# Optimization experiments

Hardware: AMD Instinct MI355X
Metric: run time of the kernel (lower is better)

## Reference

```python
import jax, jax.numpy as jnp
import numpy as np

N, E, F_IN, HID, H1, H3, NC, G = 10000, 160000, 256, 128, 5, 3, 10, 64
NEG_SLOPE = 0.2  # PyG GATConv default


def _segment_softmax(e, seg, num_segments):
    # e: [E, H] edge logits, softmax over edges sharing the same destination
    m = jax.ops.segment_max(e, seg, num_segments=num_segments)  # [N, H]
    ex = jnp.exp(e - m[seg])
    s = jax.ops.segment_sum(ex, seg, num_segments=num_segments)
    return ex / (s[seg] + 1e-16)


def _gat_conv(x, src, dst, n, W, a_src, a_dst, b, concat):
    H, C = a_src.shape
    h = (x @ W).reshape(n, H, C)                 # per-head projected features
    al_s = (h * a_src).sum(-1)                   # [N, H]
    al_d = (h * a_dst).sum(-1)                   # [N, H]
    e = jax.nn.leaky_relu(al_s[src] + al_d[dst], NEG_SLOPE)   # [E, H]
    alpha = _segment_softmax(e, dst, n)
    out = jax.ops.segment_sum(alpha[:, :, None] * h[src], dst, num_segments=n)  # [N,H,C]
    out = out.reshape(n, H * C) if concat else out.mean(axis=1)
    return out + b


def setup_inputs():
    key = jax.random.key(0)
    ks = jax.random.split(key, 16)
    s = 0.1
    return {
        "x": jax.random.normal(ks[0], (N, F_IN), jnp.float32),
        "edge_index": jax.random.randint(ks[1], (2, E), 0, N),
        "batch": jnp.sort(jax.random.randint(ks[2], (N,), 0, G)),
        "W1": jax.random.normal(ks[3], (F_IN, H1 * HID), jnp.float32) * s,
        "a1s": jax.random.normal(ks[4], (H1, HID), jnp.float32) * s,
        "a1d": jax.random.normal(ks[5], (H1, HID), jnp.float32) * s,
        "b1": jnp.zeros((H1 * HID,), jnp.float32),
        "W2": jax.random.normal(ks[6], (H1 * HID, H1 * HID), jnp.float32) * s,
        "a2s": jax.random.normal(ks[7], (H1, HID), jnp.float32) * s,
        "a2d": jax.random.normal(ks[8], (H1, HID), jnp.float32) * s,
        "b2": jnp.zeros((H1 * HID,), jnp.float32),
        "W3": jax.random.normal(ks[9], (H1 * HID, H3 * HID), jnp.float32) * s,
        "a3s": jax.random.normal(ks[10], (H3, HID), jnp.float32) * s,
        "a3d": jax.random.normal(ks[11], (H3, HID), jnp.float32) * s,
        "b3": jnp.zeros((HID,), jnp.float32),
        "Wc": jax.random.normal(ks[12], (HID, NC), jnp.float32) * s,
        "bc": jnp.zeros((NC,), jnp.float32),
    }


def reference(x, edge_index, batch, W1, a1s, a1d, b1, W2, a2s, a2d, b2,
              W3, a3s, a3d, b3, Wc, bc):
    n = x.shape[0]
    # add self-loops (PyG GATConv default)
    loop = jnp.arange(n)
    src = jnp.concatenate([edge_index[0], loop])
    dst = jnp.concatenate([edge_index[1], loop])
    # dropout omitted: inference/eval mode
    x1 = jax.nn.elu(_gat_conv(x, src, dst, n, W1, a1s, a1d, b1, True))
    h = _gat_conv(x1, src, dst, n, W2, a2s, a2d, b2, True)
    x2 = jax.nn.elu(x1 + h)
    x3 = _gat_conv(x2, src, dst, n, W3, a3s, a3d, b3, False)  # concat=False -> head mean
    counts = jax.ops.segment_sum(jnp.ones((n,), x3.dtype), batch, num_segments=G)
    pooled = jax.ops.segment_sum(x3, batch, num_segments=G) / jnp.maximum(counts, 1.0)[:, None]
    logits = pooled @ Wc + bc
    return logits, jax.nn.log_softmax(logits, axis=1)
```

## Files before the change

kernel.cpp:

```cpp
#include <hip/hip_runtime.h>
#include <math.h>

#define NNODES 10000
#define NPAD   10112
#define NEDGES 160000
#define ETOT   170000
#define FIN    256
#define HIDC   128
#define NH1    5
#define NH3    3
#define NCLS   10
#define NG     64

typedef unsigned short u16;
typedef unsigned int   u32;
typedef __attribute__((ext_vector_type(8))) short short8;
typedef __attribute__((ext_vector_type(4))) float f32x4;

__device__ __forceinline__ u16 f2b(float f) {
    union { float f; u32 u; } v; v.f = f;
    u32 r = v.u + 0x7FFF + ((v.u >> 16) & 1);
    return (u16)(r >> 16);
}
__device__ __forceinline__ float b2f(u16 b) {
    union { u32 u; float f; } v; v.u = ((u32)b) << 16; return v.f;
}

__device__ __forceinline__ float wave_sum(float v) {
    #pragma unroll
    for (int m = 32; m; m >>= 1) v += __shfl_xor(v, m);
    return v;
}

__global__ void k_init(int* __restrict__ deg, int* __restrict__ cursor, int n) {
    int i = blockIdx.x * blockDim.x + threadIdx.x;
    if (i < n) { deg[i] = 1; cursor[i] = 0; }
}

__global__ void k_count(const int* __restrict__ dstv, int* __restrict__ deg, int E) {
    int e = blockIdx.x * blockDim.x + threadIdx.x;
    if (e < E) atomicAdd(&deg[dstv[e]], 1);
}

__global__ void k_scan(const int* __restrict__ deg, int* __restrict__ offs, int n) {
    __shared__ int wsum[4];
    __shared__ int carry_s;
    const int lane = threadIdx.x & 63, wave = threadIdx.x >> 6;
    if (threadIdx.x == 0) carry_s = 0;
    __syncthreads();
    for (int base = 0; base < n; base += 256) {
        int i = base + (int)threadIdx.x;
        int v = (i < n) ? deg[i] : 0;
        int xs = v;
        #pragma unroll
        for (int d = 1; d < 64; d <<= 1) {
            int y = __shfl_up(xs, d);
            if (lane >= d) xs += y;
        }
        if (lane == 63) wsum[wave] = xs;
        __syncthreads();
        int wadd = 0;
        for (int w = 0; w < wave; ++w) wadd += wsum[w];
        int incl = carry_s + wadd + xs;
        if (i < n) offs[i + 1] = incl;
        __syncthreads();
        if (threadIdx.x == 255) carry_s = incl;
        __syncthreads();
    }
    if (threadIdx.x == 0) offs[0] = 0;
}

__global__ void k_scatter(const int* __restrict__ srcv, const int* __restrict__ dstv,
                          const int* __restrict__ offs, int* __restrict__ cursor,
                          int* __restrict__ csr, int* __restrict__ dstc, int E, int N) {
    int e = blockIdx.x * blockDim.x + threadIdx.x;
    if (e >= E + N) return;
    int s, d;
    if (e < E) { s = srcv[e]; d = dstv[e]; }
    else       { s = d = e - E; }
    int pos = offs[d] + atomicAdd(&cursor[d], 1);
    csr[pos] = s;
    dstc[pos] = d;
}

__global__ void k_f2b4(const float4* __restrict__ X, uint2* __restrict__ Y, int n4) {
    int i = blockIdx.x * blockDim.x + threadIdx.x;
    if (i >= n4) return;
    float4 v = X[i];
    uint2 o;
    o.x = (u32)f2b(v.x) | ((u32)f2b(v.y) << 16);
    o.y = (u32)f2b(v.z) | ((u32)f2b(v.w) << 16);
    Y[i] = o;
}

__global__ void k_wt(const float* __restrict__ W, u16* __restrict__ Wt, int K, int Nw) {
    int i = blockIdx.x * blockDim.x + threadIdx.x;
    if (i >= K * Nw) return;
    int k = i / Nw, n = i - k * Nw;
    Wt[(size_t)n * K + k] = f2b(W[i]);
}

__global__ __launch_bounds__(256) void k_gemm_mfma(const u16* __restrict__ A,
                                                   const u16* __restrict__ Bt,
                                                   u16* __restrict__ C,
                                                   const float* __restrict__ a_s,
                                                   const float* __restrict__ a_d,
                                                   float* __restrict__ als,
                                                   float* __restrict__ ald,
                                                   int M, int K) {
    __shared__ __align__(16) u16 As[64 * 64];
    __shared__ __align__(16) u16 Bs[128 * 64];
    __shared__ float sAls[4][64];
    __shared__ float sAld[4][64];
    const int t = threadIdx.x;
    const int lane = t & 63, wave = t >> 6;
    const int row0 = blockIdx.x * 64;
    const int head = blockIdx.y;
    const int wn = wave * 32;
    const int frow = lane & 15, quad = lane >> 4;

    f32x4 acc[4][2];
    #pragma unroll
    for (int i = 0; i < 4; ++i)
        #pragma unroll
        for (int j = 0; j < 2; ++j)
            acc[i][j] = (f32x4){0.f, 0.f, 0.f, 0.f};

    const int srow = t >> 3;
    const int sg   = t & 7;

    short8 avec[2], bvec[4];
    #pragma unroll
    for (int i = 0; i < 2; ++i) {
        int r = srow + i * 32;
        avec[i] = *(const short8*)(A + (size_t)(row0 + r) * K + sg * 8);
    }
    #pragma unroll
    for (int i = 0; i < 4; ++i) {
        int r = srow + i * 32;
        bvec[i] = *(const short8*)(Bt + (size_t)(head * 128 + r) * K + sg * 8);
    }

    for (int k0 = 0; k0 < K; k0 += 64) {
        __syncthreads();
        #pragma unroll
        for (int i = 0; i < 2; ++i) {
            int r = srow + i * 32;
            *(short8*)(As + r * 64 + (sg ^ (r & 7)) * 8) = avec[i];
        }
        #pragma unroll
        for (int i = 0; i < 4; ++i) {
            int r = srow + i * 32;
            *(short8*)(Bs + r * 64 + (sg ^ (r & 7)) * 8) = bvec[i];
        }
        __syncthreads();
        if (k0 + 64 < K) {
            #pragma unroll
            for (int i = 0; i < 2; ++i) {
                int r = srow + i * 32;
                avec[i] = *(const short8*)(A + (size_t)(row0 + r) * K + k0 + 64 + sg * 8);
            }
            #pragma unroll
            for (int i = 0; i < 4; ++i) {
                int r = srow + i * 32;
                bvec[i] = *(const short8*)(Bt + (size_t)(head * 128 + r) * K + k0 + 64 + sg * 8);
            }
        }
        #pragma unroll
        for (int c = 0; c < 2; ++c) {
            short8 af[4], bfv[2];
            #pragma unroll
            for (int mi = 0; mi < 4; ++mi) {
                int rr = mi * 16 + frow;
                int g = (c * 4 + quad) ^ (rr & 7);
                af[mi] = *(const short8*)(As + rr * 64 + g * 8);
            }
            #pragma unroll
            for (int ni = 0; ni < 2; ++ni) {
                int rr = wn + ni * 16 + frow;
                int g = (c * 4 + quad) ^ (rr & 7);
                bfv[ni] = *(const short8*)(Bs + rr * 64 + g * 8);
            }
            #pragma unroll
            for (int mi = 0; mi < 4; ++mi)
                #pragma unroll
                for (int ni = 0; ni < 2; ++ni)
                    acc[mi][ni] = __builtin_amdgcn_mfma_f32_16x16x32_bf16(
                        af[mi], bfv[ni], acc[mi][ni], 0, 0, 0);
        }
    }
    u16* Ch = C + (size_t)head * NPAD * HIDC;
    float ps[16], pd[16];
    #pragma unroll
    for (int i = 0; i < 16; ++i) { ps[i] = 0.f; pd[i] = 0.f; }
    #pragma unroll
    for (int ni = 0; ni < 2; ++ni) {
        int col = wn + ni * 16 + frow;
        float as_c = a_s[head * HIDC + col];
        float ad_c = a_d[head * HIDC + col];
        #pragma unroll
        for (int mi = 0; mi < 4; ++mi) {
            #pragma unroll
            for (int r = 0; r < 4; ++r) {
                int row = row0 + mi * 16 + quad * 4 + r;
                u16 hb = f2b(acc[mi][ni][r]);
                if (row < M) Ch[(size_t)row * HIDC + col] = hb;
                float hv = b2f(hb);
                ps[mi * 4 + r] = fmaf(hv, as_c, ps[mi * 4 + r]);
                pd[mi * 4 + r] = fmaf(hv, ad_c, pd[mi * 4 + r]);
            }
        }
    }
    #pragma unroll
    for (int i = 0; i < 16; ++i) {
        #pragma unroll
        for (int msk = 1; msk < 16; msk <<= 1) {
            ps[i] += __shfl_xor(ps[i], msk);
            pd[i] += __shfl_xor(pd[i], msk);
        }
    }
    if (frow == 0) {
        #pragma unroll
        for (int mi = 0; mi < 4; ++mi)
            #pragma unroll
            for (int r = 0; r < 4; ++r) {
                sAls[wave][mi * 16 + quad * 4 + r] = ps[mi * 4 + r];
                sAld[wave][mi * 16 + quad * 4 + r] = pd[mi * 4 + r];
            }
    }
    __syncthreads();
    if (t < 64) {
        int row = row0 + t;
        if (row < M) {
            float vs = sAls[0][t] + sAls[1][t] + sAls[2][t] + sAls[3][t];
            float vd = sAld[0][t] + sAld[1][t] + sAld[2][t] + sAld[3][t];
            als[(size_t)head * NNODES + row] = vs;
            ald[(size_t)head * NNODES + row] = vd;
        }
    }
}

__global__ void k_elog(const float* __restrict__ als, const float* __restrict__ ald,
                       const int* __restrict__ csr, const int* __restrict__ dstc,
                       float* __restrict__ elog, int total) {
    int i = blockIdx.x * blockDim.x + threadIdx.x;
    if (i >= total) return;
    int hh = i / ETOT, e = i - hh * ETOT;
    int s = csr[e], d = dstc[e];
    float v = als[(size_t)hh * NNODES + s] + ald[(size_t)hh * NNODES + d];
    v = v > 0.f ? v : 0.2f * v;
    elog[i] = __expf(v);
}

template <int MODE>
__global__ __launch_bounds__(256) void k_agg(const u16* __restrict__ h,
                                             const float* __restrict__ elog,
                                             const int* __restrict__ offs,
                                             const int* __restrict__ csr,
                                             const float* __restrict__ bias,
                                             const float* __restrict__ residf,
                                             u16* __restrict__ outbf,
                                             float* __restrict__ outf, int NHtot) {
    const int b = blockIdx.x * 4 + (threadIdx.x >> 6);
    if (b >= NHtot) return;
    const int head = b / NNODES, n = b - head * NNODES;
    const int lane = threadIdx.x & 63;
    const int grp = lane >> 4;
    const int fl  = lane & 15;
    const int e0 = offs[n], e1 = offs[n + 1];
    const float* el = elog + (size_t)head * ETOT;
    const u16* hh = h + (size_t)head * NPAD * HIDC;

    float acc[8];
    #pragma unroll
    for (int i = 0; i < 8; ++i) acc[i] = 0.f;
    float wsum = 0.f;
    int e = e0 + grp;
    for (; e + 4 < e1; e += 8) {
        float w0 = el[e];
        float w1 = el[e + 4];
        int s0 = csr[e];
        int s1 = csr[e + 4];
        short8 hv0 = *(const short8*)(hh + (size_t)s0 * HIDC + fl * 8);
        short8 hv1 = *(const short8*)(hh + (size_t)s1 * HIDC + fl * 8);
        wsum += w0;
        #pragma unroll
        for (int i = 0; i < 8; ++i)
            acc[i] = fmaf(w0, b2f((u16)hv0[i]), acc[i]);
        wsum += w1;
        #pragma unroll
        for (int i = 0; i < 8; ++i)
            acc[i] = fmaf(w1, b2f((u16)hv1[i]), acc[i]);
    }
    for (; e < e1; e += 4) {
        float w = el[e];
        int s = csr[e];
        short8 hv = *(const short8*)(hh + (size_t)s * HIDC + fl * 8);
        wsum += w;
        #pragma unroll
        for (int i = 0; i < 8; ++i)
            acc[i] = fmaf(w, b2f((u16)hv[i]), acc[i]);
    }
    #pragma unroll
    for (int i = 0; i < 8; ++i) {
        acc[i] += __shfl_xor(acc[i], 16);
        acc[i] += __shfl_xor(acc[i], 32);
    }
    wsum += __shfl_xor(wsum, 16);
    wsum += __shfl_xor(wsum, 32);
    const float inv = 1.f / (wsum + 1e-16f);
    const int j0 = grp * 2;
    float v0 = acc[j0] * inv;
    float v1 = acc[j0 + 1] * inv;
    const int fo = fl * 8 + j0;
    if (MODE == 2) {
        *(float2*)(outf + ((size_t)head * NNODES + n) * HIDC + fo) = make_float2(v0, v1);
    } else {
        const int f0 = head * HIDC + fo;
        if (MODE == 1) {
            float2 r = *(const float2*)(residf + (size_t)n * 640 + f0);
            v0 = r.x + v0;
            v1 = r.y + v1;
        }
        v0 += bias[f0];
        v1 += bias[f0 + 1];
        v0 = v0 > 0.f ? v0 : expm1f(v0);
        v1 = v1 > 0.f ? v1 : expm1f(v1);
        *(u32*)(outbf + (size_t)n * 640 + f0) = (u32)f2b(v0) | ((u32)f2b(v1) << 16);
        if (MODE == 0)
            *(float2*)(outf + (size_t)n * 640 + f0) = make_float2(v0, v1);
    }
}

__global__ void k_mean_bias(const float* __restrict__ agg, const float* __restrict__ b,
                            float* __restrict__ o, int total) {
    int i = blockIdx.x * blockDim.x + threadIdx.x;
    if (i >= total) return;
    int n = i >> 7, c = i & 127;
    float v = (agg[((size_t)0 * NNODES + n) * HIDC + c] +
               agg[((size_t)1 * NNODES + n) * HIDC + c] +
               agg[((size_t)2 * NNODES + n) * HIDC + c]) * (1.f / 3.f) + b[c];
    o[i] = v;
}

__global__ void k_pool_zero(float* __restrict__ pooled, float* __restrict__ cnts) {
    int i = blockIdx.x * blockDim.x + threadIdx.x;
    if (i < NG * HIDC) pooled[i] = 0.f;
    if (i < NG) cnts[i] = 0.f;
}

#define PCHUNK 16
__global__ __launch_bounds__(128) void k_pool_chunk(const float* __restrict__ x3,
                                                    const int* __restrict__ batch,
                                                    float* __restrict__ pooled,
                                                    float* __restrict__ cnts, int N) {
    const int c  = threadIdx.x;
    const int n0 = blockIdx.x * PCHUNK;
    const int n1 = min(n0 + PCHUNK, N);
    int   cur = batch[n0];
    float acc = 0.f;
    int   cnt = 0;
    for (int n = n0; n < n1; ++n) {
        int g = batch[n];
        if (g != cur) {
            atomicAdd(&pooled[cur * HIDC + c], acc);
            if (c == 0) atomicAdd(&cnts[cur], (float)cnt);
            acc = 0.f; cnt = 0; cur = g;
        }
        acc += x3[(size_t)n * HIDC + c];
        ++cnt;
    }
    atomicAdd(&pooled[cur * HIDC + c], acc);
    if (c == 0) atomicAdd(&cnts[cur], (float)cnt);
}

__global__ void k_head(const float* __restrict__ pooled, const float* __restrict__ cnts,
                       const float* __restrict__ Wc, const float* __restrict__ bc,
                       float* __restrict__ out) {
    __shared__ float lg[NG][NCLS];
    int tid = threadIdx.x;
    if (tid < NG * NCLS) {
        int g = tid / NCLS, c = tid % NCLS;
        float invc = 1.f / fmaxf(cnts[g], 1.f);
        float s = bc[c];
        for (int k = 0; k < HIDC; ++k)
            s = fmaf(pooled[g * HIDC + k] * invc, Wc[k * NCLS + c], s);
        lg[g][c] = s;
        out[tid] = s;
    }
    __syncthreads();
    if (tid < NG * NCLS) {
        int g = tid / NCLS, c = tid % NCLS;
        float m = -1e30f;
        for (int j = 0; j < NCLS; ++j) m = fmaxf(m, lg[g][j]);
        float se = 0.f;
        for (int j = 0; j < NCLS; ++j) se += __expf(lg[g][j] - m);
        out[NG * NCLS + tid] = lg[g][c] - m - __logf(se);
    }
}

extern "C" void kernel_launch(void* const* d_in, const int* in_sizes, int n_in,
                              void* d_out, int out_size, void* d_ws, size_t ws_size,
                              hipStream_t stream) {
    const float* x   = (const float*)d_in[0];
    const int*   ei  = (const int*)d_in[1];
    const int*   bat = (const int*)d_in[2];
    const float* W1  = (const float*)d_in[3];
    const float* a1s = (const float*)d_in[4];
    const float* a1d = (const float*)d_in[5];
    const float* b1  = (const float*)d_in[6];
    const float* W2  = (const float*)d_in[7];
    const float* a2s = (const float*)d_in[8];
    const float* a2d = (const float*)d_in[9];
    const float* b2  = (const float*)d_in[10];
    const float* W3  = (const float*)d_in[11];
    const float* a3s = (const float*)d_in[12];
    const float* a3d = (const float*)d_in[13];
    const float* b3  = (const float*)d_in[14];
    const float* Wc  = (const float*)d_in[15];
    const float* bc  = (const float*)d_in[16];
    float* out = (float*)d_out;

    char* p = (char*)d_ws;
    auto alloc = [&](size_t bytes) -> char* {
        char* r = p; p += (bytes + 255) & ~(size_t)255; return r;
    };
    u16*   xbf    = (u16*)alloc((size_t)NPAD * FIN * 2);
    u16*   x1bf   = (u16*)alloc((size_t)NPAD * 640 * 2);
    u16*   x2bf   = (u16*)alloc((size_t)NPAD * 640 * 2);
    u16*   hbf    = (u16*)alloc((size_t)NH1 * NPAD * HIDC * 2);
    u16*   W1t    = (u16*)alloc((size_t)640 * FIN * 2);
    u16*   W2t    = (u16*)alloc((size_t)640 * 640 * 2);
    u16*   W3t    = (u16*)alloc((size_t)384 * 640 * 2);
    float* x1f    = (float*)alloc((size_t)NNODES * 640 * 4);
    float* agg    = (float*)alloc((size_t)NH3 * NNODES * HIDC * 4);
    float* x3     = (float*)alloc((size_t)NNODES * HIDC * 4);
    float* als    = (float*)alloc((size_t)NNODES * NH1 * 4);
    float* ald    = (float*)alloc((size_t)NNODES * NH1 * 4);
    float* elog   = (float*)alloc((size_t)NH1 * ETOT * 4);
    float* pooled = (float*)alloc(NG * HIDC * 4);
    float* cnts   = (float*)alloc(NG * 4);
    int*   offs   = (int*)alloc((NNODES + 1) * 4);
    int*   cursor = (int*)alloc(NNODES * 4);
    int*   deg    = (int*)alloc(NNODES * 4);
    int*   csr    = (int*)alloc((size_t)ETOT * 4);
    int*   dstc   = (int*)alloc((size_t)ETOT * 4);

    const int* srcv = ei;
    const int* dstv = ei + NEDGES;

    k_init<<<(NNODES + 255) / 256, 256, 0, stream>>>(deg, cursor, NNODES);
    k_count<<<(NEDGES + 255) / 256, 256, 0, stream>>>(dstv, deg, NEDGES);
    k_scan<<<1, 256, 0, stream>>>(deg, offs, NNODES);
    k_scatter<<<(ETOT + 255) / 256, 256, 0, stream>>>(srcv, dstv, offs, cursor,
                                                      csr, dstc, NEDGES, NNODES);

    k_f2b4<<<(NNODES * FIN / 4 + 255) / 256, 256, 0, stream>>>((const float4*)x,
                                                               (uint2*)xbf, NNODES * FIN / 4);
    k_wt<<<(FIN * 640 + 255) / 256, 256, 0, stream>>>(W1, W1t, FIN, 640);
    k_wt<<<(640 * 640 + 255) / 256, 256, 0, stream>>>(W2, W2t, 640, 640);
    k_wt<<<(640 * 384 + 255) / 256, 256, 0, stream>>>(W3, W3t, 640, 384);

    const int MB = NPAD / 64;

    k_gemm_mfma<<<dim3(MB, 5), 256, 0, stream>>>(xbf, W1t, hbf, a1s, a1d, als, ald,
                                                 NNODES, FIN);
    k_elog<<<(NH1 * ETOT + 255) / 256, 256, 0, stream>>>(als, ald, csr, dstc, elog,
                                                         NH1 * ETOT);
    k_agg<0><<<(NNODES * NH1 + 3) / 4, 256, 0, stream>>>(hbf, elog, offs, csr, b1,
                                                         (const float*)nullptr, x1bf,
                                                         x1f, NNODES * NH1);
    k_gemm_mfma<<<dim3(MB, 5), 256, 0, stream>>>(x1bf, W2t, hbf, a2s, a2d, als, ald,
                                                 NNODES, 640);
    k_elog<<<(NH1 * ETOT + 255) / 256, 256, 0, stream>>>(als, ald, csr, dstc, elog,
                                                         NH1 * ETOT);
    k_agg<1><<<(NNODES * NH1 + 3) / 4, 256, 0, stream>>>(hbf, elog, offs, csr, b2,
                                                         x1f, x2bf,
                                                         (float*)nullptr, NNODES * NH1);
    k_gemm_mfma<<<dim3(MB, 3), 256, 0, stream>>>(x2bf, W3t, hbf, a3s, a3d, als, ald,
                                                 NNODES, 640);
    k_elog<<<(NH3 * ETOT + 255) / 256, 256, 0, stream>>>(als, ald, csr, dstc, elog,
                                                         NH3 * ETOT);
    k_agg<2><<<(NNODES * NH3 + 3) / 4, 256, 0, stream>>>(hbf, elog, offs, csr,
                                                         (const float*)nullptr,
                                                         (const float*)nullptr,
                                                         (u16*)nullptr, agg,
                                                         NNODES * NH3);
    k_mean_bias<<<(NNODES * HIDC + 255) / 256, 256, 0, stream>>>(agg, b3, x3,
                                                                 NNODES * HIDC);
    k_pool_zero<<<(NG * HIDC + 255) / 256, 256, 0, stream>>>(pooled, cnts);
    k_pool_chunk<<<(NNODES + PCHUNK - 1) / PCHUNK, 128, 0, stream>>>(x3, bat, pooled,
                                                                     cnts, NNODES);
    k_head<<<1, 640, 0, stream>>>(pooled, cnts, Wc, bc, out);
}
```

Baseline: 342.9 us.

## Fuse prep kernels, fold head-mean into pooling, widen scan, unroll aggregation

Merges the input conversion, three weight transposes and pool zeroing into a single prep launch. It also removes the separate mean+bias kernel by averaging the three heads inside the pooling kernel and adding the bias in the head kernel, which avoids writing and re-reading the x3 buffer. The single-block scan now uses 1024 threads to cut the number of serial iterations. The aggregation loop is unrolled to 16 edges per iteration for more memory-level parallelism, at the cost of higher register pressure.

```diff
diff --git a/kernel.cpp b/kernel.cpp
--- a/kernel.cpp
+++ b/kernel.cpp
@@ -26,12 +26,6 @@
     union { u32 u; float f; } v; v.u = ((u32)b) << 16; return v.f;
 }
 
-__device__ __forceinline__ float wave_sum(float v) {
-    #pragma unroll
-    for (int m = 32; m; m >>= 1) v += __shfl_xor(v, m);
-    return v;
-}
-
 __global__ void k_init(int* __restrict__ deg, int* __restrict__ cursor, int n) {
     int i = blockIdx.x * blockDim.x + threadIdx.x;
     if (i < n) { deg[i] = 1; cursor[i] = 0; }
@@ -42,13 +36,14 @@
     if (e < E) atomicAdd(&deg[dstv[e]], 1);
 }
 
-__global__ void k_scan(const int* __restrict__ deg, int* __restrict__ offs, int n) {
-    __shared__ int wsum[4];
+__global__ __launch_bounds__(1024) void k_scan(const int* __restrict__ deg,
+                                               int* __restrict__ offs, int n) {
+    __shared__ int wsum[16];
     __shared__ int carry_s;
     const int lane = threadIdx.x & 63, wave = threadIdx.x >> 6;
     if (threadIdx.x == 0) carry_s = 0;
     __syncthreads();
-    for (int base = 0; base < n; base += 256) {
+    for (int base = 0; base < n; base += 1024) {
         int i = base + (int)threadIdx.x;
         int v = (i < n) ? deg[i] : 0;
         int xs = v;
@@ -64,7 +59,7 @@
         int incl = carry_s + wadd + xs;
         if (i < n) offs[i + 1] = incl;
         __syncthreads();
-        if (threadIdx.x == 255) carry_s = incl;
+        if (threadIdx.x == 1023) carry_s = incl;
         __syncthreads();
     }
     if (threadIdx.x == 0) offs[0] = 0;
@@ -83,21 +78,48 @@
     dstc[pos] = d;
 }
 
-__global__ void k_f2b4(const float4* __restrict__ X, uint2* __restrict__ Y, int n4) {
+#define N4    (NNODES * FIN / 4)
+#define J1    (FIN * 640)
+#define J2    (640 * 640)
+#define J3    (640 * 384)
+#define JPOOL (NG * HIDC + NG)
+#define JTOT  (N4 + J1 + J2 + J3 + JPOOL)
+__global__ void k_prep(const float4* __restrict__ X, uint2* __restrict__ Y,
+                       const float* __restrict__ W1, u16* __restrict__ W1t,
+                       const float* __restrict__ W2, u16* __restrict__ W2t,
+                       const float* __restrict__ W3, u16* __restrict__ W3t,
+                       float* __restrict__ pooled, float* __restrict__ cnts) {
     int i = blockIdx.x * blockDim.x + threadIdx.x;
-    if (i >= n4) return;
-    float4 v = X[i];
-    uint2 o;
-    o.x = (u32)f2b(v.x) | ((u32)f2b(v.y) << 16);
-    o.y = (u32)f2b(v.z) | ((u32)f2b(v.w) << 16);
-    Y[i] = o;
-}
-
-__global__ void k_wt(const float* __restrict__ W, u16* __restrict__ Wt, int K, int Nw) {
-    int i = blockIdx.x * blockDim.x + threadIdx.x;
-    if (i >= K * Nw) return;
-    int k = i / Nw, n = i - k * Nw;
-    Wt[(size_t)n * K + k] = f2b(W[i]);
+    if (i < N4) {
+        float4 v = X[i];
+        uint2 o;
+        o.x = (u32)f2b(v.x) | ((u32)f2b(v.y) << 16);
+        o.y = (u32)f2b(v.z) | ((u32)f2b(v.w) << 16);
+        Y[i] = o;
+        return;
+    }
+    i -= N4;
+    if (i < J1) {
+        int k = i / 640, n = i - k * 640;
+        W1t[(size_t)n * FIN + k] = f2b(W1[i]);
+        return;
+    }
+    i -= J1;
+    if (i < J2) {
+        int k = i / 640, n = i - k * 640;
+        W2t[(size_t)n * 640 + k] = f2b(W2[i]);
+        return;
+    }
+    i -= J2;
+    if (i < J3) {
+        int k = i / 384, n = i - k * 384;
+        W3t[(size_t)n * 640 + k] = f2b(W3[i]);
+        return;
+    }
+    i -= J3;
+    if (i < NG * HIDC) { pooled[i] = 0.f; return; }
+    i -= NG * HIDC;
+    if (i < NG) cnts[i] = 0.f;
 }
 
 __global__ __launch_bounds__(256) void k_gemm_mfma(const u16* __restrict__ A,
@@ -276,21 +298,37 @@
     for (int i = 0; i < 8; ++i) acc[i] = 0.f;
     float wsum = 0.f;
     int e = e0 + grp;
+    for (; e + 12 < e1; e += 16) {
+        float w0 = el[e], w1 = el[e + 4], w2 = el[e + 8], w3 = el[e + 12];
+        int s0 = csr[e], s1 = csr[e + 4], s2 = csr[e + 8], s3 = csr[e + 12];
+        short8 hv0 = *(const short8*)(hh + (size_t)s0 * HIDC + fl * 8);
+        short8 hv1 = *(const short8*)(hh + (size_t)s1 * HIDC + fl * 8);
+        short8 hv2 = *(const short8*)(hh + (size_t)s2 * HIDC + fl * 8);
+        short8 hv3 = *(const short8*)(hh + (size_t)s3 * HIDC + fl * 8);
+        wsum += w0;
+        #pragma unroll
+        for (int i = 0; i < 8; ++i) acc[i] = fmaf(w0, b2f((u16)hv0[i]), acc[i]);
+        wsum += w1;
+        #pragma unroll
+        for (int i = 0; i < 8; ++i) acc[i] = fmaf(w1, b2f((u16)hv1[i]), acc[i]);
+        wsum += w2;
+        #pragma unroll
+        for (int i = 0; i < 8; ++i) acc[i] = fmaf(w2, b2f((u16)hv2[i]), acc[i]);
+        wsum += w3;
+        #pragma unroll
+        for (int i = 0; i < 8; ++i) acc[i] = fmaf(w3, b2f((u16)hv3[i]), acc[i]);
+    }
     for (; e + 4 < e1; e += 8) {
-        float w0 = el[e];
-        float w1 = el[e + 4];
-        int s0 = csr[e];
-        int s1 = csr[e + 4];
+        float w0 = el[e], w1 = el[e + 4];
+        int s0 = csr[e], s1 = csr[e + 4];
         short8 hv0 = *(const short8*)(hh + (size_t)s0 * HIDC + fl * 8);
         short8 hv1 = *(const short8*)(hh + (size_t)s1 * HIDC + fl * 8);
         wsum += w0;
         #pragma unroll
-        for (int i = 0; i < 8; ++i)
-            acc[i] = fmaf(w0, b2f((u16)hv0[i]), acc[i]);
+        for (int i = 0; i < 8; ++i) acc[i] = fmaf(w0, b2f((u16)hv0[i]), acc[i]);
         wsum += w1;
         #pragma unroll
-        for (int i = 0; i < 8; ++i)
-            acc[i] = fmaf(w1, b2f((u16)hv1[i]), acc[i]);
+        for (int i = 0; i < 8; ++i) acc[i] = fmaf(w1, b2f((u16)hv1[i]), acc[i]);
     }
     for (; e < e1; e += 4) {
         float w = el[e];
@@ -298,8 +336,7 @@
         short8 hv = *(const short8*)(hh + (size_t)s * HIDC + fl * 8);
         wsum += w;
         #pragma unroll
-        for (int i = 0; i < 8; ++i)
-            acc[i] = fmaf(w, b2f((u16)hv[i]), acc[i]);
+        for (int i = 0; i < 8; ++i) acc[i] = fmaf(w, b2f((u16)hv[i]), acc[i]);
     }
     #pragma unroll
     for (int i = 0; i < 8; ++i) {
@@ -332,25 +369,8 @@
     }
 }
 
-__global__ void k_mean_bias(const float* __restrict__ agg, const float* __restrict__ b,
-                            float* __restrict__ o, int total) {
-    int i = blockIdx.x * blockDim.x + threadIdx.x;
-    if (i >= total) return;
-    int n = i >> 7, c = i & 127;
-    float v = (agg[((size_t)0 * NNODES + n) * HIDC + c] +
-               agg[((size_t)1 * NNODES + n) * HIDC + c] +
-               agg[((size_t)2 * NNODES + n) * HIDC + c]) * (1.f / 3.f) + b[c];
-    o[i] = v;
-}
-
-__global__ void k_pool_zero(float* __restrict__ pooled, float* __restrict__ cnts) {
-    int i = blockIdx.x * blockDim.x + threadIdx.x;
-    if (i < NG * HIDC) pooled[i] = 0.f;
-    if (i < NG) cnts[i] = 0.f;
-}
-
 #define PCHUNK 16
-__global__ __launch_bounds__(128) void k_pool_chunk(const float* __restrict__ x3,
+__global__ __launch_bounds__(128) void k_pool_chunk(const float* __restrict__ agg,
                                                     const int* __restrict__ batch,
                                                     float* __restrict__ pooled,
                                                     float* __restrict__ cnts, int N) {
@@ -367,7 +387,10 @@
             if (c == 0) atomicAdd(&cnts[cur], (float)cnt);
             acc = 0.f; cnt = 0; cur = g;
         }
-        acc += x3[(size_t)n * HIDC + c];
+        float v = (agg[((size_t)0 * NNODES + n) * HIDC + c] +
+                   agg[((size_t)1 * NNODES + n) * HIDC + c] +
+                   agg[((size_t)2 * NNODES + n) * HIDC + c]) * (1.f / 3.f);
+        acc += v;
         ++cnt;
     }
     atomicAdd(&pooled[cur * HIDC + c], acc);
@@ -375,16 +398,18 @@
 }
 
 __global__ void k_head(const float* __restrict__ pooled, const float* __restrict__ cnts,
-                       const float* __restrict__ Wc, const float* __restrict__ bc,
-                       float* __restrict__ out) {
+                       const float* __restrict__ b3, const float* __restrict__ Wc,
+                       const float* __restrict__ bc, float* __restrict__ out) {
     __shared__ float lg[NG][NCLS];
     int tid = threadIdx.x;
     if (tid < NG * NCLS) {
         int g = tid / NCLS, c = tid % NCLS;
         float invc = 1.f / fmaxf(cnts[g], 1.f);
         float s = bc[c];
-        for (int k = 0; k < HIDC; ++k)
-            s = fmaf(pooled[g * HIDC + k] * invc, Wc[k * NCLS + c], s);
+        for (int k = 0; k < HIDC; ++k) {
+            float val = pooled[g * HIDC + k] * invc + b3[k];
+            s = fmaf(val, Wc[k * NCLS + c], s);
+        }
         lg[g][c] = s;
         out[tid] = s;
     }
@@ -434,7 +459,6 @@
     u16*   W3t    = (u16*)alloc((size_t)384 * 640 * 2);
     float* x1f    = (float*)alloc((size_t)NNODES * 640 * 4);
     float* agg    = (float*)alloc((size_t)NH3 * NNODES * HIDC * 4);
-    float* x3     = (float*)alloc((size_t)NNODES * HIDC * 4);
     float* als    = (float*)alloc((size_t)NNODES * NH1 * 4);
     float* ald    = (float*)alloc((size_t)NNODES * NH1 * 4);
     float* elog   = (float*)alloc((size_t)NH1 * ETOT * 4);
@@ -451,15 +475,13 @@
 
     k_init<<<(NNODES + 255) / 256, 256, 0, stream>>>(deg, cursor, NNODES);
     k_count<<<(NEDGES + 255) / 256, 256, 0, stream>>>(dstv, deg, NEDGES);
-    k_scan<<<1, 256, 0, stream>>>(deg, offs, NNODES);
+    k_scan<<<1, 1024, 0, stream>>>(deg, offs, NNODES);
     k_scatter<<<(ETOT + 255) / 256, 256, 0, stream>>>(srcv, dstv, offs, cursor,
                                                       csr, dstc, NEDGES, NNODES);
 
-    k_f2b4<<<(NNODES * FIN / 4 + 255) / 256, 256, 0, stream>>>((const float4*)x,
-                                                               (uint2*)xbf, NNODES * FIN / 4);
-    k_wt<<<(FIN * 640 + 255) / 256, 256, 0, stream>>>(W1, W1t, FIN, 640);
-    k_wt<<<(640 * 640 + 255) / 256, 256, 0, stream>>>(W2, W2t, 640, 640);
-    k_wt<<<(640 * 384 + 255) / 256, 256, 0, stream>>>(W3, W3t, 640, 384);
+    k_prep<<<(JTOT + 255) / 256, 256, 0, stream>>>((const float4*)x, (uint2*)xbf,
+                                                   W1, W1t, W2, W2t, W3, W3t,
+                                                   pooled, cnts);
 
     const int MB = NPAD / 64;
 
@@ -486,10 +508,7 @@
                                                          (const float*)nullptr,
                                                          (u16*)nullptr, agg,
                                                          NNODES * NH3);
-    k_mean_bias<<<(NNODES * HIDC + 255) / 256, 256, 0, stream>>>(agg, b3, x3,
-                                                                 NNODES * HIDC);
-    k_pool_zero<<<(NG * HIDC + 255) / 256, 256, 0, stream>>>(pooled, cnts);
-    k_pool_chunk<<<(NNODES + PCHUNK - 1) / PCHUNK, 128, 0, stream>>>(x3, bat, pooled,
+    k_pool_chunk<<<(NNODES + PCHUNK - 1) / PCHUNK, 128, 0, stream>>>(agg, bat, pooled,
                                                                      cnts, NNODES);
-    k_head<<<1, 640, 0, stream>>>(pooled, cnts, Wc, bc, out);
-}
+    k_head<<<1, 640, 0, stream>>>(pooled, cnts, b3, Wc, bc, out);
+}
```

Result: faster. 302.2 us (-11.9%).
